# Kernel tuning notes

Measured on AMD Instinct MI355X. Metric: run time of the kernel, lower is better.

## Reference

```python
import jax, jax.numpy as jnp
import numpy as np

L, H, D, FF = 6, 16, 768, 3072
B, N = 4, 1023
HD = D // H  # 48
EPS = 1e-5


def _layernorm(x, w, b):
    m = jnp.mean(x, axis=-1, keepdims=True)
    v = jnp.mean((x - m) ** 2, axis=-1, keepdims=True)
    return (x - m) / jnp.sqrt(v + EPS) * w + b


def setup_inputs() -> dict:
    key = jax.random.key(0)
    ks = jax.random.split(key, 10)
    ratio = 2.0 ** (-8.0 / H)
    slopes = np.array([ratio ** (i + 1) for i in range(H)], dtype=np.float32)
    return {
        "cls_tokens": jax.random.normal(ks[0], (B, N, D), jnp.float32),
        "cls_token": jax.random.normal(ks[1], (1, 1, D), jnp.float32) * 0.02,
        "log_slopes": jnp.log(jnp.asarray(slopes)),
        "Wqkv": jax.random.normal(ks[2], (L, 3 * D, D), jnp.float32) * 0.02,
        "Wo": jax.random.normal(ks[3], (L, D, D), jnp.float32) * 0.02,
        "Wg": jax.random.normal(ks[4], (L, FF, D), jnp.float32) * 0.02,
        "Wu": jax.random.normal(ks[5], (L, FF, D), jnp.float32) * 0.02,
        "Wd": jax.random.normal(ks[6], (L, D, FF), jnp.float32) * 0.02,
        "ln1_w": jnp.ones((L, D), jnp.float32),
        "ln1_b": jnp.zeros((L, D), jnp.float32),
        "ln2_w": jnp.ones((L, D), jnp.float32),
        "ln2_b": jnp.zeros((L, D), jnp.float32),
        "fin_w": jnp.ones((D,), jnp.float32),
        "fin_b": jnp.zeros((D,), jnp.float32),
    }


def reference(cls_tokens, cls_token, log_slopes, Wqkv, Wo, Wg, Wu, Wd,
              ln1_w, ln1_b, ln2_w, ln2_b, fin_w, fin_b):
    b, n, dmodel = cls_tokens.shape
    S = n + 1
    # learnable ALiBi: -exp(log_slope) * |i - j|, shape (H, S, S)
    pos = jnp.arange(S)
    dist = jnp.abs(pos[None, :] - pos[:, None]).astype(cls_tokens.dtype)
    bias = -(jnp.exp(log_slopes)[:, None, None] * dist[None, :, :])

    x = jnp.concatenate([jnp.broadcast_to(cls_token, (b, 1, dmodel)), cls_tokens], axis=1)
    scale = 1.0 / jnp.sqrt(jnp.asarray(HD, x.dtype))

    for l in range(L):
        h = _layernorm(x, ln1_w[l], ln1_b[l])
        qkv = jnp.einsum('bsd,ed->bse', h, Wqkv[l]).reshape(b, S, 3, H, HD)
        qkv = qkv.transpose(2, 0, 3, 1, 4)  # (3, B, H, S, hd)
        q, k, v = qkv[0], qkv[1], qkv[2]
        scores = jnp.einsum('bhqd,bhkd->bhqk', q, k) * scale + bias[None]
        attn = jax.nn.softmax(scores, axis=-1)
        o = jnp.einsum('bhqk,bhkd->bhqd', attn, v)
        o = o.transpose(0, 2, 1, 3).reshape(b, S, dmodel)
        x = x + jnp.einsum('bsd,ed->bse', o, Wo[l])
        h = _layernorm(x, ln2_w[l], ln2_b[l])
        gate = jax.nn.silu(jnp.einsum('bsd,fd->bsf', h, Wg[l]))
        up = jnp.einsum('bsd,fd->bsf', h, Wu[l])
        x = x + jnp.einsum('bsf,df->bsd', gate * up, Wd[l])

    return _layernorm(x[:, 0, :], fin_w, fin_b)
```

## Files before the change

kernel.cpp:

```cpp
#include <hip/hip_runtime.h>
#include <hip/hip_bf16.h>

#define LNUM 6
#define HNUM 16
#define DMODEL 768
#define FFDIM 3072
#define BATCH 4
#define NTOK 1023
#define SEQ 1024
#define HD 48
#define EPS 1e-5f

typedef __hip_bfloat16 bf16;

__device__ __forceinline__ unsigned short f2bf_raw(float f) {
  bf16 h = __float2bfloat16(f);
  union { bf16 h; unsigned short s; } u; u.h = h; return u.s;
}
__device__ __forceinline__ float bflo(unsigned int u) { return __uint_as_float(u << 16); }
__device__ __forceinline__ float bfhi(unsigned int u) { return __uint_as_float(u & 0xffff0000u); }

__global__ __launch_bounds__(256) void concat_kernel(
    const float* __restrict__ cls_tokens, const float* __restrict__ cls_token,
    float* __restrict__ x) {
  size_t i = (size_t)blockIdx.x * blockDim.x + threadIdx.x;
  const size_t total = (size_t)BATCH * SEQ * DMODEL;
  if (i >= total) return;
  int d = (int)(i % DMODEL);
  size_t bs = i / DMODEL;
  int s = (int)(bs % SEQ);
  int b = (int)(bs / SEQ);
  float v;
  if (s == 0) v = cls_token[d];
  else v = cls_tokens[((size_t)b * NTOK + (s - 1)) * DMODEL + d];
  x[i] = v;
}

#define W_QKV4  442368
#define W_O4    147456
#define W_FF4   589824
__global__ __launch_bounds__(256) void convert_w_kernel(
    const float* __restrict__ wqkv, const float* __restrict__ wo,
    const float* __restrict__ wg, const float* __restrict__ wu,
    const float* __restrict__ wd, bf16* __restrict__ dst) {
  size_t i4 = (size_t)blockIdx.x * 256 + threadIdx.x;
  size_t off4 = i4;
  const float* src;
  if (off4 < W_QKV4) src = wqkv;
  else { off4 -= W_QKV4;
    if (off4 < W_O4) src = wo;
    else { off4 -= W_O4;
      if (off4 < W_FF4) src = wg;
      else { off4 -= W_FF4;
        if (off4 < W_FF4) src = wu;
        else { off4 -= W_FF4; src = wd; } } } }
  float4 v = ((const float4*)src)[off4];
  ushort4 o;
  o.x = f2bf_raw(v.x); o.y = f2bf_raw(v.y);
  o.z = f2bf_raw(v.z); o.w = f2bf_raw(v.w);
  ((ushort4*)dst)[i4] = o;
}

__device__ __forceinline__ void st_ln(float* p, float v) { *p = v; }
__device__ __forceinline__ void st_ln(bf16* p, float v) { *p = __float2bfloat16(v); }

template <typename OUT>
__global__ __launch_bounds__(256) void ln_kernel(
    const float* __restrict__ in, OUT* __restrict__ out,
    const float* __restrict__ w, const float* __restrict__ bias,
    size_t in_stride, size_t out_stride) {
  const int row = blockIdx.x;
  const int tid = threadIdx.x;
  const float* x = in + (size_t)row * in_stride;
  OUT* y = out + (size_t)row * out_stride;

  float v0 = x[tid], v1 = x[tid + 256], v2 = x[tid + 512];
  float s = v0 + v1 + v2;
  float sq = v0 * v0 + v1 * v1 + v2 * v2;

  __shared__ float s_sum[256];
  __shared__ float s_sq[256];
  s_sum[tid] = s;
  s_sq[tid] = sq;
  __syncthreads();
  for (int off = 128; off > 0; off >>= 1) {
    if (tid < off) {
      s_sum[tid] += s_sum[tid + off];
      s_sq[tid] += s_sq[tid + off];
    }
    __syncthreads();
  }
  const float inv_d = 1.0f / (float)DMODEL;
  float mean = s_sum[0] * inv_d;
  float var = s_sq[0] * inv_d - mean * mean;
  float rstd = rsqrtf(var + EPS);

  st_ln(y + tid,       (v0 - mean) * rstd * w[tid]       + bias[tid]);
  st_ln(y + tid + 256, (v1 - mean) * rstd * w[tid + 256] + bias[tid + 256]);
  st_ln(y + tid + 512, (v2 - mean) * rstd * w[tid + 512] + bias[tid + 512]);
}

#define BM 128
#define BN 128
#define BK 32

typedef __attribute__((ext_vector_type(8))) short bfrag;
typedef __attribute__((ext_vector_type(4))) float f32x4;

__device__ __forceinline__ void async_copy16(const void* g, void* l) {
  __builtin_amdgcn_global_load_lds(
      (const __attribute__((address_space(1))) void*)g,
      (__attribute__((address_space(3))) void*)l, 16, 0, 0);
}

template <int CMODE>
__global__ __launch_bounds__(256) void gemm_bf16(
    const bf16* __restrict__ A, const bf16* __restrict__ B,
    void* __restrict__ Cv, int M, int N, int K) {
  __shared__ bf16 As[2][BM][BK];
  __shared__ bf16 Bs[2][BN][BK];

  const int tid = threadIdx.x;
  const int wave = tid >> 6;
  const int lane = tid & 63;
  const int m0 = blockIdx.y * BM;
  const int n0 = blockIdx.x * BN;
  const int wm = (wave & 1) * 64;
  const int wn = (wave >> 1) * 64;

  f32x4 acc[4][4];
#pragma unroll
  for (int i = 0; i < 4; i++)
#pragma unroll
    for (int j = 0; j < 4; j++) acc[i][j] = (f32x4)(0.f);

  const int lrow = lane >> 2;
  const int lcol = (lane & 3) * 8;
  const bf16* Ag[2]; const bf16* Bg[2];
  void *AsB[2][2], *BsB[2][2];
#pragma unroll
  for (int j = 0; j < 2; j++) {
    int c = j * 4 + wave;
    Ag[j] = A + (size_t)(m0 + c * 16 + lrow) * K + lcol;
    Bg[j] = B + (size_t)(n0 + c * 16 + lrow) * K + lcol;
#pragma unroll
    for (int bf = 0; bf < 2; bf++) {
      AsB[bf][j] = (void*)&As[bf][c * 16][0];
      BsB[bf][j] = (void*)&Bs[bf][c * 16][0];
    }
  }

#pragma unroll
  for (int j = 0; j < 2; j++) {
    async_copy16(Ag[j], AsB[0][j]);
    async_copy16(Bg[j], BsB[0][j]);
  }

  const int fr = lane & 15;
  const int fk = (lane >> 4) * 8;
  const int nk = K / BK;

  for (int ki = 0; ki < nk; ki++) {
    const int cur = ki & 1;
    __syncthreads();
    if (ki + 1 < nk) {
      const int k0 = (ki + 1) * BK;
#pragma unroll
      for (int j = 0; j < 2; j++) {
        async_copy16(Ag[j] + k0, AsB[cur ^ 1][j]);
        async_copy16(Bg[j] + k0, BsB[cur ^ 1][j]);
      }
    }
    bfrag a[4], b[4];
#pragma unroll
    for (int i = 0; i < 4; i++) {
      a[i] = *(const bfrag*)&As[cur][wm + i * 16 + fr][fk];
      b[i] = *(const bfrag*)&Bs[cur][wn + i * 16 + fr][fk];
    }
#pragma unroll
    for (int i = 0; i < 4; i++)
#pragma unroll
      for (int j = 0; j < 4; j++)
        acc[i][j] = __builtin_amdgcn_mfma_f32_16x16x32_bf16(a[i], b[j], acc[i][j], 0, 0, 0);
  }

  const int ccol = lane & 15;
  const int crow = (lane >> 4) * 4;
#pragma unroll
  for (int i = 0; i < 4; i++) {
#pragma unroll
    for (int j = 0; j < 4; j++) {
#pragma unroll
      for (int r = 0; r < 4; r++) {
        const size_t gm = m0 + wm + i * 16 + crow + r;
        const size_t gn = n0 + wn + j * 16 + ccol;
        if (CMODE == 2) {
          ((bf16*)Cv)[gm * N + gn] = __float2bfloat16(acc[i][j][r]);
        } else if (CMODE == 1) {
          float* cp = (float*)Cv + gm * N + gn;
          *cp += acc[i][j][r];
        } else {
          ((float*)Cv)[gm * N + gn] = acc[i][j][r];
        }
      }
    }
  }
}

template <int CMODE>
__global__ __launch_bounds__(256) void gemm_bf16_n64(
    const bf16* __restrict__ A, const bf16* __restrict__ B,
    void* __restrict__ Cv, int M, int N, int K) {
  __shared__ bf16 As[2][BM][BK];
  __shared__ bf16 Bs[2][64][BK];

  const int tid = threadIdx.x;
  const int wave = tid >> 6;
  const int lane = tid & 63;
  const int m0 = blockIdx.y * BM;
  const int n0 = blockIdx.x * 64;
  const int wm = (wave & 1) * 64;
  const int wn = (wave >> 1) * 32;

  f32x4 acc[4][2];
#pragma unroll
  for (int i = 0; i < 4; i++)
#pragma unroll
    for (int j = 0; j < 2; j++) acc[i][j] = (f32x4)(0.f);

  const int lrow = lane >> 2;
  const int lcol = (lane & 3) * 8;
  const bf16* Ag[2]; const bf16* Bg;
  void *AsB[2][2], *BsB[2];
#pragma unroll
  for (int j = 0; j < 2; j++) {
    int c = j * 4 + wave;
    Ag[j] = A + (size_t)(m0 + c * 16 + lrow) * K + lcol;
#pragma unroll
    for (int bf = 0; bf < 2; bf++) AsB[bf][j] = (void*)&As[bf][c * 16][0];
  }
  Bg = B + (size_t)(n0 + wave * 16 + lrow) * K + lcol;
#pragma unroll
  for (int bf = 0; bf < 2; bf++) BsB[bf] = (void*)&Bs[bf][wave * 16][0];

  async_copy16(Ag[0], AsB[0][0]);
  async_copy16(Ag[1], AsB[0][1]);
  async_copy16(Bg, BsB[0]);

  const int fr = lane & 15;
  const int fk = (lane >> 4) * 8;
  const int nk = K / BK;

  for (int ki = 0; ki < nk; ki++) {
    const int cur = ki & 1;
    __syncthreads();
    if (ki + 1 < nk) {
      const int k0 = (ki + 1) * BK;
      async_copy16(Ag[0] + k0, AsB[cur ^ 1][0]);
      async_copy16(Ag[1] + k0, AsB[cur ^ 1][1]);
      async_copy16(Bg + k0, BsB[cur ^ 1]);
    }
    bfrag a[4], b[2];
#pragma unroll
    for (int i = 0; i < 4; i++)
      a[i] = *(const bfrag*)&As[cur][wm + i * 16 + fr][fk];
#pragma unroll
    for (int j = 0; j < 2; j++)
      b[j] = *(const bfrag*)&Bs[cur][wn + j * 16 + fr][fk];
#pragma unroll
    for (int i = 0; i < 4; i++)
#pragma unroll
      for (int j = 0; j < 2; j++)
        acc[i][j] = __builtin_amdgcn_mfma_f32_16x16x32_bf16(a[i], b[j], acc[i][j], 0, 0, 0);
  }

  const int ccol = lane & 15;
  const int crow = (lane >> 4) * 4;
#pragma unroll
  for (int i = 0; i < 4; i++) {
#pragma unroll
    for (int j = 0; j < 2; j++) {
#pragma unroll
      for (int r = 0; r < 4; r++) {
        const size_t gm = m0 + wm + i * 16 + crow + r;
        const size_t gn = n0 + wn + j * 16 + ccol;
        if (CMODE == 2) {
          ((bf16*)Cv)[gm * N + gn] = __float2bfloat16(acc[i][j][r]);
        } else if (CMODE == 1) {
          float* cp = (float*)Cv + gm * N + gn;
          *cp += acc[i][j][r];
        } else {
          ((float*)Cv)[gm * N + gn] = acc[i][j][r];
        }
      }
    }
  }
}

__global__ __launch_bounds__(256) void gemm_gateup(
    const bf16* __restrict__ A, const bf16* __restrict__ Wg,
    const bf16* __restrict__ Wu, bf16* __restrict__ gu, int M, int N, int K) {
  __shared__ bf16 As[2][BM][BK];
  __shared__ bf16 Gs[2][BN][BK];
  __shared__ bf16 Us[2][BN][BK];

  const int tid = threadIdx.x;
  const int wave = tid >> 6;
  const int lane = tid & 63;
  const int m0 = blockIdx.y * BM;
  const int n0 = blockIdx.x * BN;
  const int wm = (wave & 1) * 64;
  const int wn = (wave >> 1) * 64;

  f32x4 accG[4][4], accU[4][4];
#pragma unroll
  for (int i = 0; i < 4; i++)
#pragma unroll
    for (int j = 0; j < 4; j++) { accG[i][j] = (f32x4)(0.f); accU[i][j] = (f32x4)(0.f); }

  const int lrow = lane >> 2;
  const int lcol = (lane & 3) * 8;
  const bf16 *Ag[2], *Gg[2], *Ug[2];
  void *AsB[2][2], *GsB[2][2], *UsB[2][2];
#pragma unroll
  for (int j = 0; j < 2; j++) {
    int c = j * 4 + wave;
    Ag[j] = A + (size_t)(m0 + c * 16 + lrow) * K + lcol;
    Gg[j] = Wg + (size_t)(n0 + c * 16 + lrow) * K + lcol;
    Ug[j] = Wu + (size_t)(n0 + c * 16 + lrow) * K + lcol;
#pragma unroll
    for (int bf = 0; bf < 2; bf++) {
      AsB[bf][j] = (void*)&As[bf][c * 16][0];
      GsB[bf][j] = (void*)&Gs[bf][c * 16][0];
      UsB[bf][j] = (void*)&Us[bf][c * 16][0];
    }
  }

#pragma unroll
  for (int j = 0; j < 2; j++) {
    async_copy16(Ag[j], AsB[0][j]);
    async_copy16(Gg[j], GsB[0][j]);
    async_copy16(Ug[j], UsB[0][j]);
  }

  const int fr = lane & 15;
  const int fk = (lane >> 4) * 8;
  const int nk = K / BK;

  for (int ki = 0; ki < nk; ki++) {
    const int cur = ki & 1;
    __syncthreads();
    if (ki + 1 < nk) {
      const int k0 = (ki + 1) * BK;
#pragma unroll
      for (int j = 0; j < 2; j++) {
        async_copy16(Ag[j] + k0, AsB[cur ^ 1][j]);
        async_copy16(Gg[j] + k0, GsB[cur ^ 1][j]);
        async_copy16(Ug[j] + k0, UsB[cur ^ 1][j]);
      }
    }
    bfrag a[4], g[4], u[4];
#pragma unroll
    for (int i = 0; i < 4; i++) {
      a[i] = *(const bfrag*)&As[cur][wm + i * 16 + fr][fk];
      g[i] = *(const bfrag*)&Gs[cur][wn + i * 16 + fr][fk];
      u[i] = *(const bfrag*)&Us[cur][wn + i * 16 + fr][fk];
    }
#pragma unroll
    for (int i = 0; i < 4; i++)
#pragma unroll
      for (int j = 0; j < 4; j++) {
        accG[i][j] = __builtin_amdgcn_mfma_f32_16x16x32_bf16(a[i], g[j], accG[i][j], 0, 0, 0);
        accU[i][j] = __builtin_amdgcn_mfma_f32_16x16x32_bf16(a[i], u[j], accU[i][j], 0, 0, 0);
      }
  }

  const int ccol = lane & 15;
  const int crow = (lane >> 4) * 4;
#pragma unroll
  for (int i = 0; i < 4; i++) {
#pragma unroll
    for (int j = 0; j < 4; j++) {
#pragma unroll
      for (int r = 0; r < 4; r++) {
        const size_t gm = m0 + wm + i * 16 + crow + r;
        const size_t gn = n0 + wn + j * 16 + ccol;
        const float gv = accG[i][j][r];
        const float uv = accU[i][j][r];
        const float res = gv / (1.0f + __expf(-gv)) * uv;
        gu[gm * N + gn] = __float2bfloat16(res);
      }
    }
  }
}

__global__ __launch_bounds__(256) void transpose_v(
    const bf16* __restrict__ qkv, bf16* __restrict__ vt) {
  __shared__ bf16 T[HD][64];
  const int tid = threadIdx.x;
  const int kb = blockIdx.x * 64;
  const int h = blockIdx.y;
  const int b = blockIdx.z;
  const size_t rstride = 3 * DMODEL;
  const bf16* vsrc = qkv + ((size_t)(b * SEQ + kb)) * rstride + 2 * DMODEL + h * HD;

  if (tid < 192) {
    int p = tid & 31, c = tid >> 5;
    const bf16* v0 = vsrc + (size_t)(2 * p) * rstride + c * 8;
    uint4 r0 = *(const uint4*)v0;
    uint4 r1 = *(const uint4*)(v0 + rstride);
    const unsigned int* w0 = (const unsigned int*)&r0;
    const unsigned int* w1 = (const unsigned int*)&r1;
#pragma unroll
    for (int i = 0; i < 8; i++) {
      unsigned int lo = (i & 1) ? (w0[i >> 1] >> 16) : (w0[i >> 1] & 0xffffu);
      unsigned int hi = (i & 1) ? (w1[i >> 1] >> 16) : (w1[i >> 1] & 0xffffu);
      *(unsigned int*)&T[c * 8 + i][2 * p] = lo | (hi << 16);
    }
  }
  __syncthreads();
  for (int it = tid; it < HD * 8; it += 256) {
    int d = it >> 3, c = it & 7;
    *(uint4*)(vt + ((size_t)((b * HNUM + h) * HD + d)) * SEQ + kb + c * 8) =
        *(const uint4*)&T[d][c * 8];
  }
}

#define AQT 64
#define AKT 64
#define ASTR 72

__global__ __launch_bounds__(256, 4) void attn_mfma(
    const bf16* __restrict__ qkv, const bf16* __restrict__ vt,
    const float* __restrict__ log_slopes, bf16* __restrict__ obuf) {
  __shared__ bf16 Qs[AQT][ASTR];
  __shared__ bf16 Ks[AKT][ASTR];
  __shared__ bf16 Vs[HD][ASTR];
  __shared__ bf16 Pt[AQT][ASTR];

  const int tid = threadIdx.x;
  const int wq = tid >> 6;
  const int lane = tid & 63;
  const int l15 = lane & 15;
  const int lh = lane >> 4;
  const int qb = blockIdx.x * AQT;
  const int h = blockIdx.y;
  const int b = blockIdx.z;

  const float scale = 0.14433756729740643f;
  const float slope = __expf(log_slopes[h]);
  const size_t rstride = 3 * DMODEL;
  const bf16* qbase = qkv + ((size_t)(b * SEQ + qb)) * rstride + h * HD;
  const bf16* kbase0 = qkv + ((size_t)b * SEQ) * rstride + DMODEL + h * HD;
  const bf16* vbase0 = vt + ((size_t)((b * HNUM + h) * HD)) * SEQ;

  bf16* ldst[3];
  size_t goff[3];
  bool isK[3];
#pragma unroll
  for (int j = 0; j < 3; j++) {
    int id = tid + j * 256;
    if (id < 384) {
      int r = id / 6, c = id - r * 6;
      ldst[j] = &Ks[r][c * 8];
      goff[j] = (size_t)r * rstride + c * 8;
      isK[j] = true;
    } else {
      id -= 384;
      int d = id >> 3, c = id & 7;
      ldst[j] = &Vs[d][c * 8];
      goff[j] = (size_t)d * SEQ + c * 8;
      isK[j] = false;
    }
  }

  for (int it = tid; it < AQT * 2; it += 256) {
    int r = it >> 1, c = it & 1;
    *(uint4*)&Qs[r][48 + c * 8] = make_uint4(0, 0, 0, 0);
    *(uint4*)&Ks[r][48 + c * 8] = make_uint4(0, 0, 0, 0);
  }
  for (int it = tid; it < AQT * 6; it += 256) {
    int r = it / 6, c = it - (it / 6) * 6;
    *(uint4*)&Qs[r][c * 8] = *(const uint4*)(qbase + (size_t)r * rstride + c * 8);
  }

  uint4 pre[3];
#pragma unroll
  for (int j = 0; j < 3; j++)
    pre[j] = *(const uint4*)((isK[j] ? kbase0 : vbase0) + goff[j]);

  float m[4], l[4];
  f32x4 accO[3];
#pragma unroll
  for (int r = 0; r < 4; r++) { m[r] = -1e30f; l[r] = 0.f; }
#pragma unroll
  for (int t = 0; t < 3; t++) accO[t] = (f32x4)(0.f);

  for (int kb = 0; kb < SEQ; kb += AKT) {
    __syncthreads();
#pragma unroll
    for (int j = 0; j < 3; j++) *(uint4*)ldst[j] = pre[j];
    __syncthreads();
    if (kb + AKT < SEQ) {
      const bf16* kb1 = kbase0 + (size_t)(kb + AKT) * rstride;
      const bf16* vb1 = vbase0 + (kb + AKT);
#pragma unroll
      for (int j = 0; j < 3; j++)
        pre[j] = *(const uint4*)((isK[j] ? kb1 : vb1) + goff[j]);
    }

    f32x4 accS[4];
#pragma unroll
    for (int j = 0; j < 4; j++) accS[j] = (f32x4)(0.f);
#pragma unroll
    for (int ks = 0; ks < 2; ks++) {
      bfrag a = *(const bfrag*)&Qs[wq * 16 + l15][ks * 32 + lh * 8];
#pragma unroll
      for (int j = 0; j < 4; j++) {
        bfrag bk = *(const bfrag*)&Ks[j * 16 + l15][ks * 32 + lh * 8];
        accS[j] = __builtin_amdgcn_mfma_f32_16x16x32_bf16(a, bk, accS[j], 0, 0, 0);
      }
    }

    float ps[4][4];
#pragma unroll
    for (int r = 0; r < 4; r++) {
      const int qg = qb + wq * 16 + lh * 4 + r;
      float s[4];
#pragma unroll
      for (int j = 0; j < 4; j++) {
        const int kg = kb + j * 16 + l15;
        s[j] = accS[j][r] * scale - slope * fabsf((float)(qg - kg));
      }
      float mx = fmaxf(fmaxf(s[0], s[1]), fmaxf(s[2], s[3]));
#pragma unroll
      for (int off = 1; off < 16; off <<= 1) mx = fmaxf(mx, __shfl_xor(mx, off, 64));
      const float mnew = fmaxf(m[r], mx);
      const float corr = __expf(m[r] - mnew);
      float rs = 0.f;
#pragma unroll
      for (int j = 0; j < 4; j++) {
        ps[j][r] = __expf(s[j] - mnew);
        rs += ps[j][r];
      }
#pragma unroll
      for (int off = 1; off < 16; off <<= 1) rs += __shfl_xor(rs, off, 64);
      l[r] = l[r] * corr + rs;
      m[r] = mnew;
#pragma unroll
      for (int t = 0; t < 3; t++) accO[t][r] *= corr;
    }

#pragma unroll
    for (int j = 0; j < 4; j++)
#pragma unroll
      for (int r = 0; r < 4; r++)
        Pt[wq * 16 + lh * 4 + r][j * 16 + l15] = __float2bfloat16(ps[j][r]);

#pragma unroll
    for (int ks = 0; ks < 2; ks++) {
      bfrag pa = *(const bfrag*)&Pt[wq * 16 + l15][ks * 32 + lh * 8];
#pragma unroll
      for (int t = 0; t < 3; t++) {
        bfrag vb = *(const bfrag*)&Vs[t * 16 + l15][ks * 32 + lh * 8];
        accO[t] = __builtin_amdgcn_mfma_f32_16x16x32_bf16(pa, vb, accO[t], 0, 0, 0);
      }
    }
  }

#pragma unroll
  for (int r = 0; r < 4; r++) {
    const float inv = 1.0f / l[r];
    bf16* op = obuf + ((size_t)(b * SEQ + qb + wq * 16 + lh * 4 + r)) * DMODEL + h * HD;
#pragma unroll
    for (int t = 0; t < 3; t++)
      op[t * 16 + l15] = __float2bfloat16(accO[t][r] * inv);
  }
}

extern "C" void kernel_launch(void* const* d_in, const int* in_sizes, int n_in,
                              void* d_out, int out_size, void* d_ws, size_t ws_size,
                              hipStream_t stream) {
  const float* cls_tokens = (const float*)d_in[0];
  const float* cls_token  = (const float*)d_in[1];
  const float* log_slopes = (const float*)d_in[2];
  const float* Wqkv = (const float*)d_in[3];
  const float* Wo   = (const float*)d_in[4];
  const float* Wg   = (const float*)d_in[5];
  const float* Wu   = (const float*)d_in[6];
  const float* Wd   = (const float*)d_in[7];
  const float* ln1_w = (const float*)d_in[8];
  const float* ln1_b = (const float*)d_in[9];
  const float* ln2_w = (const float*)d_in[10];
  const float* ln2_b = (const float*)d_in[11];
  const float* fin_w = (const float*)d_in[12];
  const float* fin_b = (const float*)d_in[13];
  float* out = (float*)d_out;

  const size_t ROWS = (size_t)BATCH * SEQ;
  char* wsb = (char*)d_ws;
  float* x    = (float*)(wsb);
  bf16* qkvb  = (bf16*)(wsb + 12582912);
  bf16* hb    = (bf16*)(wsb + 31457280);
  bf16* ob    = (bf16*)(wsb + 37748736);
  bf16* gub   = (bf16*)(wsb + 44040192);
  bf16* wbf   = (bf16*)(wsb + 94371840);
  bf16* vtb   = (bf16*)(wsb + 113246208);

  bf16* wqkv_b = wbf;
  bf16* wo_b   = wbf + 1769472;
  bf16* wg_b   = wbf + 2359296;
  bf16* wu_b   = wbf + 4718592;
  bf16* wd_b   = wbf + 7077888;

  {
    const size_t total = ROWS * DMODEL;
    concat_kernel<<<(int)((total + 255) / 256), 256, 0, stream>>>(cls_tokens, cls_token, x);
  }

  for (int l = 0; l < LNUM; l++) {
    convert_w_kernel<<<9216, 256, 0, stream>>>(
        Wqkv + (size_t)l * 3 * DMODEL * DMODEL, Wo + (size_t)l * DMODEL * DMODEL,
        Wg + (size_t)l * FFDIM * DMODEL, Wu + (size_t)l * FFDIM * DMODEL,
        Wd + (size_t)l * DMODEL * FFDIM, wbf);

    ln_kernel<bf16><<<(int)ROWS, 256, 0, stream>>>(
        x, hb, ln1_w + l * DMODEL, ln1_b + l * DMODEL, DMODEL, DMODEL);
    gemm_bf16<2><<<dim3(3 * DMODEL / BN, ROWS / BM), 256, 0, stream>>>(
        hb, wqkv_b, qkvb, (int)ROWS, 3 * DMODEL, DMODEL);
    transpose_v<<<dim3(SEQ / 64, HNUM, BATCH), 256, 0, stream>>>(qkvb, vtb);
    attn_mfma<<<dim3(SEQ / AQT, HNUM, BATCH), 256, 0, stream>>>(
        qkvb, vtb, log_slopes, ob);
    gemm_bf16_n64<1><<<dim3(DMODEL / 64, ROWS / BM), 256, 0, stream>>>(
        ob, wo_b, x, (int)ROWS, DMODEL, DMODEL);
    ln_kernel<bf16><<<(int)ROWS, 256, 0, stream>>>(
        x, hb, ln2_w + l * DMODEL, ln2_b + l * DMODEL, DMODEL, DMODEL);
    gemm_gateup<<<dim3(FFDIM / BN, ROWS / BM), 256, 0, stream>>>(
        hb, wg_b, wu_b, gub, (int)ROWS, FFDIM, DMODEL);
    gemm_bf16_n64<1><<<dim3(DMODEL / 64, ROWS / BM), 256, 0, stream>>>(
        gub, wd_b, x, (int)ROWS, DMODEL, FFDIM);
  }

  ln_kernel<float><<<BATCH, 256, 0, stream>>>(x, out, fin_w, fin_b,
                                              (size_t)SEQ * DMODEL, DMODEL);
}
```

Before: 1.854 ms.

## Shrink N64 GEMM tiles, remap attention grid, use DPP reductions and exp2

The narrow-N GEMM moves from 128x64 to 64x64 tiles, doubling the block count for the Wo and down projections so more CUs stay busy. The attention kernel now uses a 1D grid with a swizzled block-to-(q,h,b) mapping, exp2 with prefolded log2e constants, and DPP-based 16-lane max and sum reductions in place of shuffles. It also raises wave priority around the MFMA sections. Smaller GEMM tiles cut reuse per block, and the swizzle changes the order in which blocks touch K/V.

```diff
diff --git a/kernel.cpp b/kernel.cpp
--- a/kernel.cpp
+++ b/kernel.cpp
@@ -17,8 +17,26 @@
   bf16 h = __float2bfloat16(f);
   union { bf16 h; unsigned short s; } u; u.h = h; return u.s;
 }
-__device__ __forceinline__ float bflo(unsigned int u) { return __uint_as_float(u << 16); }
-__device__ __forceinline__ float bfhi(unsigned int u) { return __uint_as_float(u & 0xffff0000u); }
+
+template <int CTRL>
+__device__ __forceinline__ float dppf(float x) {
+  return __int_as_float(__builtin_amdgcn_update_dpp(
+      0, __float_as_int(x), CTRL, 0xf, 0xf, true));
+}
+__device__ __forceinline__ float row_max16(float x) {
+  x = fmaxf(x, dppf<0xB1>(x));
+  x = fmaxf(x, dppf<0x4E>(x));
+  x = fmaxf(x, dppf<0x124>(x));
+  x = fmaxf(x, dppf<0x128>(x));
+  return x;
+}
+__device__ __forceinline__ float row_sum16(float x) {
+  x += dppf<0xB1>(x);
+  x += dppf<0x4E>(x);
+  x += dppf<0x124>(x);
+  x += dppf<0x128>(x);
+  return x;
+}
 
 __global__ __launch_bounds__(256) void concat_kernel(
     const float* __restrict__ cls_tokens, const float* __restrict__ cls_token,
@@ -211,40 +229,35 @@
 __global__ __launch_bounds__(256) void gemm_bf16_n64(
     const bf16* __restrict__ A, const bf16* __restrict__ B,
     void* __restrict__ Cv, int M, int N, int K) {
-  __shared__ bf16 As[2][BM][BK];
+  __shared__ bf16 As[2][64][BK];
   __shared__ bf16 Bs[2][64][BK];
 
   const int tid = threadIdx.x;
   const int wave = tid >> 6;
   const int lane = tid & 63;
-  const int m0 = blockIdx.y * BM;
+  const int m0 = blockIdx.y * 64;
   const int n0 = blockIdx.x * 64;
-  const int wm = (wave & 1) * 64;
+  const int wm = (wave & 1) * 32;
   const int wn = (wave >> 1) * 32;
 
-  f32x4 acc[4][2];
-#pragma unroll
-  for (int i = 0; i < 4; i++)
+  f32x4 acc[2][2];
+#pragma unroll
+  for (int i = 0; i < 2; i++)
 #pragma unroll
     for (int j = 0; j < 2; j++) acc[i][j] = (f32x4)(0.f);
 
-  const int lrow = lane >> 2;
-  const int lcol = (lane & 3) * 8;
-  const bf16* Ag[2]; const bf16* Bg;
-  void *AsB[2][2], *BsB[2];
-#pragma unroll
-  for (int j = 0; j < 2; j++) {
-    int c = j * 4 + wave;
-    Ag[j] = A + (size_t)(m0 + c * 16 + lrow) * K + lcol;
-#pragma unroll
-    for (int bf = 0; bf < 2; bf++) AsB[bf][j] = (void*)&As[bf][c * 16][0];
-  }
-  Bg = B + (size_t)(n0 + wave * 16 + lrow) * K + lcol;
-#pragma unroll
-  for (int bf = 0; bf < 2; bf++) BsB[bf] = (void*)&Bs[bf][wave * 16][0];
-
-  async_copy16(Ag[0], AsB[0][0]);
-  async_copy16(Ag[1], AsB[0][1]);
+  const int srow = tid >> 2;
+  const int scol = (tid & 3) * 8;
+  const bf16* Ag = A + (size_t)(m0 + srow) * K + scol;
+  const bf16* Bg = B + (size_t)(n0 + srow) * K + scol;
+  void *AsB[2], *BsB[2];
+#pragma unroll
+  for (int bf = 0; bf < 2; bf++) {
+    AsB[bf] = (void*)&As[bf][srow][scol];
+    BsB[bf] = (void*)&Bs[bf][srow][scol];
+  }
+
+  async_copy16(Ag, AsB[0]);
   async_copy16(Bg, BsB[0]);
 
   const int fr = lane & 15;
@@ -256,19 +269,18 @@
     __syncthreads();
     if (ki + 1 < nk) {
       const int k0 = (ki + 1) * BK;
-      async_copy16(Ag[0] + k0, AsB[cur ^ 1][0]);
-      async_copy16(Ag[1] + k0, AsB[cur ^ 1][1]);
+      async_copy16(Ag + k0, AsB[cur ^ 1]);
       async_copy16(Bg + k0, BsB[cur ^ 1]);
     }
-    bfrag a[4], b[2];
-#pragma unroll
-    for (int i = 0; i < 4; i++)
+    bfrag a[2], b[2];
+#pragma unroll
+    for (int i = 0; i < 2; i++)
       a[i] = *(const bfrag*)&As[cur][wm + i * 16 + fr][fk];
 #pragma unroll
     for (int j = 0; j < 2; j++)
       b[j] = *(const bfrag*)&Bs[cur][wn + j * 16 + fr][fk];
 #pragma unroll
-    for (int i = 0; i < 4; i++)
+    for (int i = 0; i < 2; i++)
 #pragma unroll
       for (int j = 0; j < 2; j++)
         acc[i][j] = __builtin_amdgcn_mfma_f32_16x16x32_bf16(a[i], b[j], acc[i][j], 0, 0, 0);
@@ -277,7 +289,7 @@
   const int ccol = lane & 15;
   const int crow = (lane >> 4) * 4;
 #pragma unroll
-  for (int i = 0; i < 4; i++) {
+  for (int i = 0; i < 2; i++) {
 #pragma unroll
     for (int j = 0; j < 2; j++) {
 #pragma unroll
@@ -443,12 +455,15 @@
   const int lane = tid & 63;
   const int l15 = lane & 15;
   const int lh = lane >> 4;
-  const int qb = blockIdx.x * AQT;
-  const int h = blockIdx.y;
-  const int b = blockIdx.z;
-
-  const float scale = 0.14433756729740643f;
-  const float slope = __expf(log_slopes[h]);
+
+  const int id = blockIdx.x;
+  const int w = (id & 7) * 128 + (id >> 3);
+  const int qb = (w & 15) * AQT;
+  const int h = (w >> 4) & 15;
+  const int b = w >> 8;
+
+  const float c1 = 0.14433756729740643f * 1.4426950408889634f;
+  const float slope2 = __expf(log_slopes[h]) * 1.4426950408889634f;
   const size_t rstride = 3 * DMODEL;
   const bf16* qbase = qkv + ((size_t)(b * SEQ + qb)) * rstride + h * HD;
   const bf16* kbase0 = qkv + ((size_t)b * SEQ) * rstride + DMODEL + h * HD;
@@ -459,15 +474,15 @@
   bool isK[3];
 #pragma unroll
   for (int j = 0; j < 3; j++) {
-    int id = tid + j * 256;
-    if (id < 384) {
-      int r = id / 6, c = id - r * 6;
+    int id2 = tid + j * 256;
+    if (id2 < 384) {
+      int r = id2 / 6, c = id2 - r * 6;
       ldst[j] = &Ks[r][c * 8];
       goff[j] = (size_t)r * rstride + c * 8;
       isK[j] = true;
     } else {
-      id -= 384;
-      int d = id >> 3, c = id & 7;
+      id2 -= 384;
+      int d = id2 >> 3, c = id2 & 7;
       ldst[j] = &Vs[d][c * 8];
       goff[j] = (size_t)d * SEQ + c * 8;
       isK[j] = false;
@@ -489,10 +504,10 @@
   for (int j = 0; j < 3; j++)
     pre[j] = *(const uint4*)((isK[j] ? kbase0 : vbase0) + goff[j]);
 
-  float m[4], l[4];
+  float m_[4], l_[4];
   f32x4 accO[3];
 #pragma unroll
-  for (int r = 0; r < 4; r++) { m[r] = -1e30f; l[r] = 0.f; }
+  for (int r = 0; r < 4; r++) { m_[r] = -1e30f; l_[r] = 0.f; }
 #pragma unroll
   for (int t = 0; t < 3; t++) accO[t] = (f32x4)(0.f);
 
@@ -512,6 +527,7 @@
     f32x4 accS[4];
 #pragma unroll
     for (int j = 0; j < 4; j++) accS[j] = (f32x4)(0.f);
+    __builtin_amdgcn_s_setprio(1);
 #pragma unroll
     for (int ks = 0; ks < 2; ks++) {
       bfrag a = *(const bfrag*)&Qs[wq * 16 + l15][ks * 32 + lh * 8];
@@ -521,32 +537,31 @@
         accS[j] = __builtin_amdgcn_mfma_f32_16x16x32_bf16(a, bk, accS[j], 0, 0, 0);
       }
     }
+    __builtin_amdgcn_s_setprio(0);
 
     float ps[4][4];
 #pragma unroll
     for (int r = 0; r < 4; r++) {
-      const int qg = qb + wq * 16 + lh * 4 + r;
+      const float fq = (float)(qb + wq * 16 + lh * 4 + r);
       float s[4];
 #pragma unroll
       for (int j = 0; j < 4; j++) {
-        const int kg = kb + j * 16 + l15;
-        s[j] = accS[j][r] * scale - slope * fabsf((float)(qg - kg));
-      }
-      float mx = fmaxf(fmaxf(s[0], s[1]), fmaxf(s[2], s[3]));
-#pragma unroll
-      for (int off = 1; off < 16; off <<= 1) mx = fmaxf(mx, __shfl_xor(mx, off, 64));
-      const float mnew = fmaxf(m[r], mx);
-      const float corr = __expf(m[r] - mnew);
+        const float fk = (float)(kb + j * 16 + l15);
+        const float t = slope2 * fabsf(fq - fk);
+        s[j] = fmaf(accS[j][r], c1, -t);
+      }
+      float mx = row_max16(fmaxf(fmaxf(s[0], s[1]), fmaxf(s[2], s[3])));
+      const float mnew = fmaxf(m_[r], mx);
+      const float corr = exp2f(m_[r] - mnew);
       float rs = 0.f;
 #pragma unroll
       for (int j = 0; j < 4; j++) {
-        ps[j][r] = __expf(s[j] - mnew);
+        ps[j][r] = exp2f(s[j] - mnew);
         rs += ps[j][r];
       }
-#pragma unroll
-      for (int off = 1; off < 16; off <<= 1) rs += __shfl_xor(rs, off, 64);
-      l[r] = l[r] * corr + rs;
-      m[r] = mnew;
+      rs = row_sum16(rs);
+      l_[r] = l_[r] * corr + rs;
+      m_[r] = mnew;
 #pragma unroll
       for (int t = 0; t < 3; t++) accO[t][r] *= corr;
     }
@@ -560,17 +575,19 @@
 #pragma unroll
     for (int ks = 0; ks < 2; ks++) {
       bfrag pa = *(const bfrag*)&Pt[wq * 16 + l15][ks * 32 + lh * 8];
+      __builtin_amdgcn_s_setprio(1);
 #pragma unroll
       for (int t = 0; t < 3; t++) {
         bfrag vb = *(const bfrag*)&Vs[t * 16 + l15][ks * 32 + lh * 8];
         accO[t] = __builtin_amdgcn_mfma_f32_16x16x32_bf16(pa, vb, accO[t], 0, 0, 0);
       }
+      __builtin_amdgcn_s_setprio(0);
     }
   }
 
 #pragma unroll
   for (int r = 0; r < 4; r++) {
-    const float inv = 1.0f / l[r];
+    const float inv = 1.0f / l_[r];
     bf16* op = obuf + ((size_t)(b * SEQ + qb + wq * 16 + lh * 4 + r)) * DMODEL + h * HD;
 #pragma unroll
     for (int t = 0; t < 3; t++)
@@ -629,15 +646,15 @@
     gemm_bf16<2><<<dim3(3 * DMODEL / BN, ROWS / BM), 256, 0, stream>>>(
         hb, wqkv_b, qkvb, (int)ROWS, 3 * DMODEL, DMODEL);
     transpose_v<<<dim3(SEQ / 64, HNUM, BATCH), 256, 0, stream>>>(qkvb, vtb);
-    attn_mfma<<<dim3(SEQ / AQT, HNUM, BATCH), 256, 0, stream>>>(
+    attn_mfma<<<dim3(SEQ / AQT * HNUM * BATCH), 256, 0, stream>>>(
         qkvb, vtb, log_slopes, ob);
-    gemm_bf16_n64<1><<<dim3(DMODEL / 64, ROWS / BM), 256, 0, stream>>>(
+    gemm_bf16_n64<1><<<dim3(DMODEL / 64, ROWS / 64), 256, 0, stream>>>(
         ob, wo_b, x, (int)ROWS, DMODEL, DMODEL);
     ln_kernel<bf16><<<(int)ROWS, 256, 0, stream>>>(
         x, hb, ln2_w + l * DMODEL, ln2_b + l * DMODEL, DMODEL, DMODEL);
     gemm_gateup<<<dim3(FFDIM / BN, ROWS / BM), 256, 0, stream>>>(
         hb, wg_b, wu_b, gub, (int)ROWS, FFDIM, DMODEL);
-    gemm_bf16_n64<1><<<dim3(DMODEL / 64, ROWS / BM), 256, 0, stream>>>(
+    gemm_bf16_n64<1><<<dim3(DMODEL / 64, ROWS / 64), 256, 0, stream>>>(
         gub, wd_b, x, (int)ROWS, DMODEL, FFDIM);
   }
 
```

Result: faster. 1.754 ms (-5.4%).
